# Optimization experiments

Measured on AMD Instinct MI355X. Metric: run time of the kernel, lower is better.

## Reference

```python
import jax, jax.numpy as jnp
import numpy as np

NUM_HEADS = 12
LN_EPS = 1e-5


def _layernorm(x, w, b):
    m = jnp.mean(x, axis=-1, keepdims=True)
    v = jnp.mean(jnp.square(x - m), axis=-1, keepdims=True)
    return (x - m) * jax.lax.rsqrt(v + LN_EPS) * w + b


def setup_inputs() -> dict:
    key = jax.random.key(0)
    ks = jax.random.split(key, 6)
    B, N, C, H = 8, 1024, 768, 3072
    s = 0.02
    return {
        "x": jax.random.normal(ks[0], (B, N, C), jnp.float32),
        "ln1_w": jnp.ones((C,), jnp.float32),
        "ln1_b": jnp.zeros((C,), jnp.float32),
        "qkv_w": jax.random.normal(ks[1], (3 * C, C), jnp.float32) * s,
        "qkv_b": jnp.zeros((3 * C,), jnp.float32),
        "proj_w": jax.random.normal(ks[2], (C, C), jnp.float32) * s,
        "proj_b": jnp.zeros((C,), jnp.float32),
        "ln2_w": jnp.ones((C,), jnp.float32),
        "ln2_b": jnp.zeros((C,), jnp.float32),
        "fc1_w": jax.random.normal(ks[3], (H, C), jnp.float32) * s,
        "fc1_b": jnp.zeros((H,), jnp.float32),
        "fc2_w": jax.random.normal(ks[4], (C, H), jnp.float32) * s,
        "fc2_b": jnp.zeros((C,), jnp.float32),
    }


def reference(x, ln1_w, ln1_b, qkv_w, qkv_b, proj_w, proj_b,
              ln2_w, ln2_b, fc1_w, fc1_b, fc2_w, fc2_b):
    B, N, C = x.shape
    H = NUM_HEADS
    d = C // H
    scale = d ** (-0.5)

    # --- attention on norm1(x) (size=None path, dropout rates are 0) ---
    h = _layernorm(x, ln1_w, ln1_b)
    qkv = h @ qkv_w.T + qkv_b                      # [B,N,3C]
    qkv = qkv.reshape(B, N, 3, H, d).transpose(2, 0, 3, 1, 4)  # [3,B,H,N,d]
    q, k, v = qkv[0], qkv[1], qkv[2]
    attn = jnp.einsum('bhqd,bhkd->bhqk', q, k) * scale
    attn = jax.nn.softmax(attn, axis=-1)
    o = jnp.einsum('bhqk,bhkd->bhqd', attn, v)     # [B,H,N,d]
    o = o.transpose(0, 2, 1, 3).reshape(B, N, C)
    x_attn = o @ proj_w.T + proj_b

    # --- residual + MLP ---
    x = x + x_attn
    h2 = _layernorm(x, ln2_w, ln2_b)
    h2 = jax.nn.gelu(h2 @ fc1_w.T + fc1_b, approximate=False)
    x = x + (h2 @ fc2_w.T + fc2_b)
    return x
```

## Files before the change

kernel.cpp:

```cpp
#include <hip/hip_runtime.h>
#include <cmath>

typedef __bf16 bf16;
typedef __bf16 bf16x8 __attribute__((ext_vector_type(8)));
typedef __bf16 bf16x4 __attribute__((ext_vector_type(4)));
typedef float floatx4 __attribute__((ext_vector_type(4)));

#define MFMA16(A, B, C) __builtin_amdgcn_mfma_f32_16x16x32_bf16((A), (B), (C), 0, 0, 0)

#define GLDS16(g, l)                                                   \
  __builtin_amdgcn_global_load_lds(                                    \
      (const __attribute__((address_space(1))) void*)(g),              \
      (__attribute__((address_space(3))) void*)(l), 16, 0, 0)

__global__ __launch_bounds__(256) void pre_kernel(
    const float* __restrict__ x, const float* __restrict__ g,
    const float* __restrict__ be, bf16* __restrict__ h1,
    const float* __restrict__ s0, bf16* __restrict__ d0, int n0,
    const float* __restrict__ s1, bf16* __restrict__ d1, int n1,
    const float* __restrict__ s2, bf16* __restrict__ d2, int n2,
    const float* __restrict__ s3, bf16* __restrict__ d3, int n3) {
  int bid = blockIdx.x;
  int t = threadIdx.x;
  if (bid < 8192) {
    const float* xr = x + (size_t)bid * 768;
    float v0 = xr[t], v1 = xr[t + 256], v2 = xr[t + 512];
    float s = v0 + v1 + v2;
    float s2 = v0 * v0 + v1 * v1 + v2 * v2;
#pragma unroll
    for (int o = 1; o < 64; o <<= 1) {
      s += __shfl_xor(s, o, 64);
      s2 += __shfl_xor(s2, o, 64);
    }
    __shared__ float red[8];
    int w = t >> 6, lane = t & 63;
    if (lane == 0) { red[w] = s; red[4 + w] = s2; }
    __syncthreads();
    float ts = red[0] + red[1] + red[2] + red[3];
    float ts2 = red[4] + red[5] + red[6] + red[7];
    float mean = ts * (1.0f / 768.0f);
    float var = ts2 * (1.0f / 768.0f) - mean * mean;
    float rstd = rsqrtf(var + 1e-5f);
    bf16* orow = h1 + (size_t)bid * 768;
    orow[t]       = (bf16)((v0 - mean) * rstd * g[t]       + be[t]);
    orow[t + 256] = (bf16)((v1 - mean) * rstd * g[t + 256] + be[t + 256]);
    orow[t + 512] = (bf16)((v2 - mean) * rstd * g[t + 512] + be[t + 512]);
    return;
  }
  int i = (bid - 8192) * 256 + t;
  const float* s;
  bf16* d;
  if (i < n0) { s = s0 + (size_t)i * 4; d = d0 + (size_t)i * 4; }
  else if ((i -= n0) < n1) { s = s1 + (size_t)i * 4; d = d1 + (size_t)i * 4; }
  else if ((i -= n1) < n2) { s = s2 + (size_t)i * 4; d = d2 + (size_t)i * 4; }
  else if ((i -= n2) < n3) { s = s3 + (size_t)i * 4; d = d3 + (size_t)i * 4; }
  else return;
  bf16x4 v;
  v[0] = (bf16)s[0]; v[1] = (bf16)s[1]; v[2] = (bf16)s[2]; v[3] = (bf16)s[3];
  *(bf16x4*)d = v;
}

__global__ __launch_bounds__(256) void ln_kernel(const float* __restrict__ x,
                                                 const float* __restrict__ g,
                                                 const float* __restrict__ be,
                                                 bf16* __restrict__ out) {
  int row = blockIdx.x;
  int t = threadIdx.x;
  const float* xr = x + (size_t)row * 768;
  float v0 = xr[t], v1 = xr[t + 256], v2 = xr[t + 512];
  float s = v0 + v1 + v2;
  float s2 = v0 * v0 + v1 * v1 + v2 * v2;
#pragma unroll
  for (int o = 1; o < 64; o <<= 1) {
    s += __shfl_xor(s, o, 64);
    s2 += __shfl_xor(s2, o, 64);
  }
  __shared__ float red[8];
  int w = t >> 6, lane = t & 63;
  if (lane == 0) { red[w] = s; red[4 + w] = s2; }
  __syncthreads();
  float ts = red[0] + red[1] + red[2] + red[3];
  float ts2 = red[4] + red[5] + red[6] + red[7];
  float mean = ts * (1.0f / 768.0f);
  float var = ts2 * (1.0f / 768.0f) - mean * mean;
  float rstd = rsqrtf(var + 1e-5f);
  bf16* orow = out + (size_t)row * 768;
  orow[t]       = (bf16)((v0 - mean) * rstd * g[t]       + be[t]);
  orow[t + 256] = (bf16)((v1 - mean) * rstd * g[t + 256] + be[t + 256]);
  orow[t + 512] = (bf16)((v2 - mean) * rstd * g[t + 512] + be[t + 512]);
}

constexpr int EP_BF16 = 0;
constexpr int EP_RES_F32 = 1;
constexpr int EP_GELU_BF16 = 2;

template <int EP, int NJ>
__global__ __launch_bounds__(256, 3) void gemm_bt(
    const bf16* __restrict__ A, const bf16* __restrict__ Bw,
    const float* __restrict__ bias, const float* __restrict__ resid,
    void* __restrict__ outp, int M, int N, int K) {
  __shared__ alignas(16) bf16 Asl[128 * 64];
  __shared__ alignas(16) bf16 Bsl[NJ * 32 * 64];
  int tid = threadIdx.x;
  int lane = tid & 63, w = tid >> 6;
  int wm = w >> 1, wn = w & 1;
  int q16 = lane & 15, quad = lane >> 4;
  int fid = blockIdx.x + gridDim.x * blockIdx.y;
  int nb = gridDim.x;
  int s = fid >> 3;
  int m0 = ((fid & 7) * (gridDim.y >> 3) + s / nb) * 128;
  int n0 = (s % nb) * (NJ * 32);

  floatx4 acc[4][NJ];
#pragma unroll
  for (int i = 0; i < 4; i++)
#pragma unroll
    for (int j = 0; j < NJ; j++) acc[i][j] = (floatx4){0.f, 0.f, 0.f, 0.f};

  int rIn = lane >> 3;
  int cg = (lane & 7) ^ rIn;
  const bf16* ag[4];
  const bf16* bg[NJ];
#pragma unroll
  for (int q = 0; q < 4; q++)
    ag[q] = A + (size_t)(m0 + (w * 4 + q) * 8 + rIn) * K + cg * 8;
#pragma unroll
  for (int q = 0; q < NJ; q++)
    bg[q] = Bw + (size_t)(n0 + (w * NJ + q) * 8 + rIn) * K + cg * 8;
  bf16* la = &Asl[w * 2048];
  bf16* lb = &Bsl[w * NJ * 512];

  int msel = q16 & 7;
  int offA[2][4], offB[2][NJ];
#pragma unroll
  for (int ks = 0; ks < 2; ks++) {
#pragma unroll
    for (int i = 0; i < 4; i++)
      offA[ks][i] = (wm * 64 + i * 16 + q16) * 64 + (((ks * 4 + quad) ^ msel)) * 8;
#pragma unroll
    for (int j = 0; j < NJ; j++)
      offB[ks][j] = (wn * 16 * NJ + j * 16 + q16) * 64 + (((ks * 4 + quad) ^ msel)) * 8;
  }

  for (int k0 = 0; k0 < K; k0 += 64) {
    __syncthreads();
#pragma unroll
    for (int q = 0; q < 4; q++) {
      GLDS16(ag[q], la + q * 512);
      ag[q] += 64;
    }
#pragma unroll
    for (int q = 0; q < NJ; q++) {
      GLDS16(bg[q], lb + q * 512);
      bg[q] += 64;
    }
    __syncthreads();
#pragma unroll
    for (int ks = 0; ks < 2; ks++) {
      bf16x8 af[4], bfr[NJ];
#pragma unroll
      for (int i = 0; i < 4; i++) af[i] = *(const bf16x8*)&Asl[offA[ks][i]];
#pragma unroll
      for (int j = 0; j < NJ; j++) bfr[j] = *(const bf16x8*)&Bsl[offB[ks][j]];
#pragma unroll
      for (int i = 0; i < 4; i++)
#pragma unroll
        for (int j = 0; j < NJ; j++) acc[i][j] = MFMA16(af[i], bfr[j], acc[i][j]);
    }
  }

#pragma unroll
  for (int i = 0; i < 4; i++) {
#pragma unroll
    for (int j = 0; j < NJ; j++) {
#pragma unroll
      for (int r = 0; r < 4; r++) {
        int m = m0 + wm * 64 + i * 16 + quad * 4 + r;
        int n = n0 + wn * 16 * NJ + j * 16 + q16;
        size_t idx = (size_t)m * N + n;
        float v = acc[i][j][r] + bias[n];
        if constexpr (EP == EP_BF16) {
          ((bf16*)outp)[idx] = (bf16)v;
        } else if constexpr (EP == EP_RES_F32) {
          ((float*)outp)[idx] = v + resid[idx];
        } else {
          float u = v * (2.3022083f + 0.1029443f * v * v);
          float e = __builtin_amdgcn_exp2f(-u);
          float gv = v * __builtin_amdgcn_rcpf(1.0f + e);
          ((bf16*)outp)[idx] = (bf16)gv;
        }
      }
    }
  }
}

__global__ __launch_bounds__(256, 3) void attn_kernel(const bf16* __restrict__ qkv,
                                                      bf16* __restrict__ o) {
  __shared__ alignas(16) bf16 Kl[2][32 * 64];
  __shared__ alignas(16) bf16 Vt[2][64 * 40];
  __shared__ alignas(16) bf16 Pl[4][2][16 * 68];
  int tid = threadIdx.x;
  int lane = tid & 63, w = tid >> 6;
  int q16 = lane & 15, quad = lane >> 4;
  int f = blockIdx.x;
  int xcd = f & 7, idx = f >> 3;
  int b = xcd, h = idx % 12;
  int qbase = (idx / 12) * 128 + w * 32;

  bf16x8 qf[2][2];
#pragma unroll
  for (int qt = 0; qt < 2; qt++)
#pragma unroll
    for (int c = 0; c < 2; c++)
      qf[qt][c] = *(const bf16x8*)(qkv +
          (size_t)(b * 1024 + qbase + qt * 16 + q16) * 2304 + h * 64 +
          c * 32 + quad * 8);

  int kkey = w * 8 + (lane >> 3);
  int kchunk = (lane & 7) ^ (lane >> 3);
  const bf16* kg0 = qkv + (size_t)(b * 1024 + kkey) * 2304 + 768 + h * 64 +
                    kchunk * 8;
  const bf16* kg1 = kg0 + 32 * 2304;
  bf16* kd0 = &Kl[0][w * 512];
  bf16* kd1 = &Kl[1][w * 512];

  int kr = tid >> 3;
  int kcb = (tid & 7) * 8;
  const bf16* vg0 = qkv + (size_t)(b * 1024 + kr) * 2304 + 1536 + h * 64 + kcb;
  const bf16* vg1 = vg0 + 32 * 2304;
  int vt_idx[8];
#pragma unroll
  for (int e = 0; e < 8; e++)
    vt_idx[e] = ((((kcb + e) * 5) + (kr >> 3)) ^ (tid & 7)) * 8 + (kr & 7);

  int koff[2][2];
#pragma unroll
  for (int nc = 0; nc < 2; nc++)
#pragma unroll
    for (int ck = 0; ck < 2; ck++) {
      int key = nc * 16 + q16;
      koff[nc][ck] = (key * 8 + ((ck * 4 + quad) ^ (key & 7))) * 8;
    }
  int voff[4];
#pragma unroll
  for (int dc = 0; dc < 4; dc++) {
    int d = dc * 16 + q16;
    voff[dc] = ((d * 5 + quad) ^ ((d >> 3) & 7)) * 8;
  }
  const bf16* pread = &Pl[w][0][q16 * 68 + quad * 8];
  int pw_base = (quad * 4) * 68 + q16;

  float l_[2][4];
  floatx4 oacc[2][4];
#pragma unroll
  for (int qt = 0; qt < 2; qt++)
#pragma unroll
    for (int r = 0; r < 4; r++) l_[qt][r] = 0.f;
#pragma unroll
  for (int qt = 0; qt < 2; qt++)
#pragma unroll
    for (int dc = 0; dc < 4; dc++) oacc[qt][dc] = (floatx4){0.f, 0.f, 0.f, 0.f};

  for (int kt = 0; kt < 16; kt++) {
    __syncthreads();
    GLDS16(kg0, kd0);
    GLDS16(kg1, kd1);
    bf16x8 vv0 = *(const bf16x8*)vg0;
    bf16x8 vv1 = *(const bf16x8*)vg1;
    kg0 += 64 * 2304; kg1 += 64 * 2304;
    vg0 += 64 * 2304; vg1 += 64 * 2304;
#pragma unroll
    for (int e = 0; e < 8; e++) Vt[0][vt_idx[e]] = vv0[e];
#pragma unroll
    for (int e = 0; e < 8; e++) Vt[1][vt_idx[e]] = vv1[e];
    __syncthreads();

    bf16x8 kf[4][2];
#pragma unroll
    for (int nc = 0; nc < 4; nc++)
#pragma unroll
      for (int ck = 0; ck < 2; ck++)
        kf[nc][ck] = *(const bf16x8*)&Kl[nc >> 1][koff[nc & 1][ck]];

#pragma unroll
    for (int qt = 0; qt < 2; qt++) {
#pragma unroll
      for (int nc = 0; nc < 4; nc++) {
        floatx4 z = (floatx4){0.f, 0.f, 0.f, 0.f};
        z = MFMA16(qf[qt][0], kf[nc][0], z);
        z = MFMA16(qf[qt][1], kf[nc][1], z);
#pragma unroll
        for (int r = 0; r < 4; r++) {
          float p = __builtin_amdgcn_exp2f(z[r] * 0.18033688011f);
          l_[qt][r] += p;
          Pl[w][qt][pw_base + r * 68 + nc * 16] = (bf16)p;
        }
      }
    }

    bf16x8 vf[2][4];
#pragma unroll
    for (int kh = 0; kh < 2; kh++)
#pragma unroll
      for (int dc = 0; dc < 4; dc++)
        vf[kh][dc] = *(const bf16x8*)&Vt[kh][voff[dc]];
#pragma unroll
    for (int qt = 0; qt < 2; qt++) {
#pragma unroll
      for (int kh = 0; kh < 2; kh++) {
        bf16x8 pf = *(const bf16x8*)(pread + qt * 1088 + kh * 32);
#pragma unroll
        for (int dc = 0; dc < 4; dc++)
          oacc[qt][dc] = MFMA16(pf, vf[kh][dc], oacc[qt][dc]);
      }
    }
  }

#pragma unroll
  for (int qt = 0; qt < 2; qt++) {
    bf16* op = o + (size_t)(b * 1024 + qbase + qt * 16) * 768 + h * 64;
#pragma unroll
    for (int r = 0; r < 4; r++) {
      float s = l_[qt][r];
#pragma unroll
      for (int off = 1; off < 16; off <<= 1) s += __shfl_xor(s, off, 16);
      float inv = 1.0f / s;
#pragma unroll
      for (int dc = 0; dc < 4; dc++)
        op[(size_t)(quad * 4 + r) * 768 + dc * 16 + q16] =
            (bf16)(oacc[qt][dc][r] * inv);
    }
  }
}

extern "C" void kernel_launch(void* const* d_in, const int* in_sizes, int n_in,
                              void* d_out, int out_size, void* d_ws, size_t ws_size,
                              hipStream_t stream) {
  (void)in_sizes; (void)n_in; (void)out_size; (void)ws_size;
  const float* x      = (const float*)d_in[0];
  const float* ln1_w  = (const float*)d_in[1];
  const float* ln1_b  = (const float*)d_in[2];
  const float* qkv_w  = (const float*)d_in[3];
  const float* qkv_b  = (const float*)d_in[4];
  const float* proj_w = (const float*)d_in[5];
  const float* proj_b = (const float*)d_in[6];
  const float* ln2_w  = (const float*)d_in[7];
  const float* ln2_b  = (const float*)d_in[8];
  const float* fc1_w  = (const float*)d_in[9];
  const float* fc1_b  = (const float*)d_in[10];
  const float* fc2_w  = (const float*)d_in[11];
  const float* fc2_b  = (const float*)d_in[12];

  char* ws = (char*)d_ws;
  size_t off = 0;
  auto alloc = [&](size_t bytes) {
    void* p = ws + off;
    off += (bytes + 255) & ~(size_t)255;
    return p;
  };
  bf16* wq  = (bf16*)alloc((size_t)2304 * 768 * 2);
  bf16* wp  = (bf16*)alloc((size_t)768 * 768 * 2);
  bf16* wf1 = (bf16*)alloc((size_t)3072 * 768 * 2);
  bf16* wf2 = (bf16*)alloc((size_t)768 * 3072 * 2);
  bf16* slotA = (bf16*)alloc((size_t)8192 * 768 * 2);
  bf16* slotB = (bf16*)alloc((size_t)8192 * 3072 * 2);
  float* x1 = (float*)alloc((size_t)8192 * 768 * 4);

  bf16* h1 = slotA;
  bf16* qkvb = slotB;
  bf16* ob = slotA;
  bf16* h2 = slotA;
  bf16* hm = slotB;

  pre_kernel<<<8192 + 6912, 256, 0, stream>>>(
      x, ln1_w, ln1_b, h1,
      qkv_w, wq, 2304 * 768 / 4, proj_w, wp, 768 * 768 / 4,
      fc1_w, wf1, 3072 * 768 / 4, fc2_w, wf2, 768 * 3072 / 4);

  gemm_bt<EP_BF16, 4><<<dim3(18, 64), 256, 0, stream>>>(
      h1, wq, qkv_b, nullptr, qkvb, 8192, 2304, 768);
  attn_kernel<<<768, 256, 0, stream>>>(qkvb, ob);
  gemm_bt<EP_RES_F32, 2><<<dim3(12, 64), 256, 0, stream>>>(
      ob, wp, proj_b, x, x1, 8192, 768, 768);
  ln_kernel<<<8192, 256, 0, stream>>>(x1, ln2_w, ln2_b, h2);
  gemm_bt<EP_GELU_BF16, 4><<<dim3(24, 64), 256, 0, stream>>>(
      h2, wf1, fc1_b, nullptr, hm, 8192, 3072, 768);
  gemm_bt<EP_RES_F32, 2><<<dim3(12, 64), 256, 0, stream>>>(
      hm, wf2, fc2_b, x1, (float*)d_out, 8192, 768, 3072);
}
```

Before: 332.2 us.

## Double-buffer K/V tiles in attention and prefetch next tile during compute

```diff
diff --git a/kernel.cpp b/kernel.cpp
--- a/kernel.cpp
+++ b/kernel.cpp
@@ -198,14 +198,13 @@
                                                       bf16* __restrict__ o) {
   __shared__ alignas(16) bf16 Kl[2][32 * 64];
   __shared__ alignas(16) bf16 Vt[2][64 * 40];
-  __shared__ alignas(16) bf16 Pl[4][2][16 * 68];
+  __shared__ alignas(16) bf16 Pl[4][2][16 * 40];
   int tid = threadIdx.x;
   int lane = tid & 63, w = tid >> 6;
   int q16 = lane & 15, quad = lane >> 4;
-  int f = blockIdx.x;
-  int xcd = f & 7, idx = f >> 3;
-  int b = xcd, h = idx % 12;
-  int qbase = (idx / 12) * 128 + w * 32;
+  int b = blockIdx.y / 12, h = blockIdx.y % 12;
+  int qbase = blockIdx.x * 128 + w * 32;
+  const int KS = 32 * 2304;
 
   bf16x8 qf[2][2];
 #pragma unroll
@@ -218,20 +217,17 @@
 
   int kkey = w * 8 + (lane >> 3);
   int kchunk = (lane & 7) ^ (lane >> 3);
-  const bf16* kg0 = qkv + (size_t)(b * 1024 + kkey) * 2304 + 768 + h * 64 +
-                    kchunk * 8;
-  const bf16* kg1 = kg0 + 32 * 2304;
-  bf16* kd0 = &Kl[0][w * 512];
-  bf16* kd1 = &Kl[1][w * 512];
+  const bf16* kg = qkv + (size_t)(b * 1024 + kkey) * 2304 + 768 + h * 64 +
+                   kchunk * 8;
+  bf16* kd[2] = {&Kl[0][w * 512], &Kl[1][w * 512]};
 
   int kr = tid >> 3;
   int kcb = (tid & 7) * 8;
-  const bf16* vg0 = qkv + (size_t)(b * 1024 + kr) * 2304 + 1536 + h * 64 + kcb;
-  const bf16* vg1 = vg0 + 32 * 2304;
+  const bf16* vg = qkv + (size_t)(b * 1024 + kr) * 2304 + 1536 + h * 64 + kcb;
   int vt_idx[8];
 #pragma unroll
   for (int e = 0; e < 8; e++)
-    vt_idx[e] = ((((kcb + e) * 5) + (kr >> 3)) ^ (tid & 7)) * 8 + (kr & 7);
+    vt_idx[e] = ((((kcb + e) * 5) + w) ^ (tid & 7)) * 8 + (kr & 7);
 
   int koff[2][2];
 #pragma unroll
@@ -247,8 +243,8 @@
     int d = dc * 16 + q16;
     voff[dc] = ((d * 5 + quad) ^ ((d >> 3) & 7)) * 8;
   }
-  const bf16* pread = &Pl[w][0][q16 * 68 + quad * 8];
-  int pw_base = (quad * 4) * 68 + q16;
+  const bf16* pread = &Pl[w][0][q16 * 40 + quad * 8];
+  int pw_base = (quad * 4) * 40 + q16;
 
   float l_[2][4];
   floatx4 oacc[2][4];
@@ -261,31 +257,40 @@
 #pragma unroll
     for (int dc = 0; dc < 4; dc++) oacc[qt][dc] = (floatx4){0.f, 0.f, 0.f, 0.f};
 
-  for (int kt = 0; kt < 16; kt++) {
+  GLDS16(kg, kd[0]);
+  kg += KS;
+  bf16x8 vv = *(const bf16x8*)vg;
+  vg += KS;
+#pragma unroll
+  for (int e = 0; e < 8; e++) Vt[0][vt_idx[e]] = vv[e];
+  vv = *(const bf16x8*)vg;
+  vg += KS;
+
+  for (int kt = 0; kt < 32; kt++) {
+    int cur = kt & 1, nxt = cur ^ 1;
     __syncthreads();
-    GLDS16(kg0, kd0);
-    GLDS16(kg1, kd1);
-    bf16x8 vv0 = *(const bf16x8*)vg0;
-    bf16x8 vv1 = *(const bf16x8*)vg1;
-    kg0 += 64 * 2304; kg1 += 64 * 2304;
-    vg0 += 64 * 2304; vg1 += 64 * 2304;
-#pragma unroll
-    for (int e = 0; e < 8; e++) Vt[0][vt_idx[e]] = vv0[e];
-#pragma unroll
-    for (int e = 0; e < 8; e++) Vt[1][vt_idx[e]] = vv1[e];
-    __syncthreads();
-
-    bf16x8 kf[4][2];
-#pragma unroll
-    for (int nc = 0; nc < 4; nc++)
+    if (kt < 31) {
+      GLDS16(kg, kd[nxt]);
+      kg += KS;
+#pragma unroll
+      for (int e = 0; e < 8; e++) Vt[nxt][vt_idx[e]] = vv[e];
+      if (kt < 30) {
+        vv = *(const bf16x8*)vg;
+        vg += KS;
+      }
+    }
+
+    bf16x8 kf[2][2];
+#pragma unroll
+    for (int nc = 0; nc < 2; nc++)
 #pragma unroll
       for (int ck = 0; ck < 2; ck++)
-        kf[nc][ck] = *(const bf16x8*)&Kl[nc >> 1][koff[nc & 1][ck]];
+        kf[nc][ck] = *(const bf16x8*)&Kl[cur][koff[nc][ck]];
 
 #pragma unroll
     for (int qt = 0; qt < 2; qt++) {
 #pragma unroll
-      for (int nc = 0; nc < 4; nc++) {
+      for (int nc = 0; nc < 2; nc++) {
         floatx4 z = (floatx4){0.f, 0.f, 0.f, 0.f};
         z = MFMA16(qf[qt][0], kf[nc][0], z);
         z = MFMA16(qf[qt][1], kf[nc][1], z);
@@ -293,26 +298,20 @@
         for (int r = 0; r < 4; r++) {
           float p = __builtin_amdgcn_exp2f(z[r] * 0.18033688011f);
           l_[qt][r] += p;
-          Pl[w][qt][pw_base + r * 68 + nc * 16] = (bf16)p;
+          Pl[w][qt][pw_base + r * 40 + nc * 16] = (bf16)p;
         }
       }
     }
 
-    bf16x8 vf[2][4];
-#pragma unroll
-    for (int kh = 0; kh < 2; kh++)
+    bf16x8 vf[4];
+#pragma unroll
+    for (int dc = 0; dc < 4; dc++) vf[dc] = *(const bf16x8*)&Vt[cur][voff[dc]];
+#pragma unroll
+    for (int qt = 0; qt < 2; qt++) {
+      bf16x8 pf = *(const bf16x8*)(pread + qt * 640);
 #pragma unroll
       for (int dc = 0; dc < 4; dc++)
-        vf[kh][dc] = *(const bf16x8*)&Vt[kh][voff[dc]];
-#pragma unroll
-    for (int qt = 0; qt < 2; qt++) {
-#pragma unroll
-      for (int kh = 0; kh < 2; kh++) {
-        bf16x8 pf = *(const bf16x8*)(pread + qt * 1088 + kh * 32);
-#pragma unroll
-        for (int dc = 0; dc < 4; dc++)
-          oacc[qt][dc] = MFMA16(pf, vf[kh][dc], oacc[qt][dc]);
-      }
+        oacc[qt][dc] = MFMA16(pf, vf[dc], oacc[qt][dc]);
     }
   }
 
@@ -379,7 +378,7 @@
 
   gemm_bt<EP_BF16, 4><<<dim3(18, 64), 256, 0, stream>>>(
       h1, wq, qkv_b, nullptr, qkvb, 8192, 2304, 768);
-  attn_kernel<<<768, 256, 0, stream>>>(qkvb, ob);
+  attn_kernel<<<dim3(8, 96), 256, 0, stream>>>(qkvb, ob);
   gemm_bt<EP_RES_F32, 2><<<dim3(12, 64), 256, 0, stream>>>(
       ob, wp, proj_b, x, x1, 8192, 768, 768);
   ln_kernel<<<8192, 256, 0, stream>>>(x1, ln2_w, ln2_b, h2);
```

Result: faster. 320.5 us (-3.5%).
